# Kernel optimization log

Hardware: AMD Instinct MI355X
Metric: run time of the kernel (lower is better)

Reference implementation:

```python
import jax, jax.numpy as jnp
import numpy as np

WH, WW = 8, 8
N = WH * WW          # 64 tokens per window
C = 128              # channels
H = 4                # heads
HD = C // H          # head dim = 32
B = 4096             # batch * num_windows
NW = 1024            # windows per image (mask groups)
EPS = 1e-5


def _relative_position_index():
    ch = np.arange(WH)
    cw = np.arange(WW)
    coords = np.stack(np.meshgrid(ch, cw, indexing='ij'))        # (2, WH, WW)
    cf = coords.reshape(2, -1)                                    # (2, N)
    rel = cf[:, :, None] - cf[:, None, :]                         # (2, N, N)
    rel = rel.transpose(1, 2, 0).copy()                           # (N, N, 2)
    rel[:, :, 0] += WH - 1
    rel[:, :, 1] += WW - 1
    rel[:, :, 0] *= 2 * WW - 1
    return rel.sum(-1).astype(np.int32)                           # (N, N)


def setup_inputs() -> dict:
    key = jax.random.key(0)
    ks = jax.random.split(key, 12)
    s = 0.02
    tbl_size = (2 * WH - 1) * (2 * WW - 1)
    return {
        'x': jax.random.normal(ks[0], (B, N, C), jnp.float32),
        'y': jax.random.normal(ks[1], (B, N, C), jnp.float32),
        'mask': jnp.zeros((NW, N, N), jnp.float32),
        'wqkv1': jax.random.normal(ks[2], (C, 3 * C), jnp.float32) * s,
        'bqkv1': jnp.zeros((3 * C,), jnp.float32),
        'wqkv2': jax.random.normal(ks[3], (C, 3 * C), jnp.float32) * s,
        'bqkv2': jnp.zeros((3 * C,), jnp.float32),
        'tbl1': jax.random.normal(ks[4], (tbl_size, H), jnp.float32) * s,
        'tbl2': jax.random.normal(ks[5], (tbl_size, H), jnp.float32) * s,
        'wproj1': jax.random.normal(ks[6], (C, C), jnp.float32) * s,
        'bproj1': jnp.zeros((C,), jnp.float32),
        'wproj2': jax.random.normal(ks[7], (C, C), jnp.float32) * s,
        'bproj2': jnp.zeros((C,), jnp.float32),
        'g1': jnp.ones((C,), jnp.float32),
        'be1': jnp.zeros((C,), jnp.float32),
        'g2': jnp.ones((C,), jnp.float32),
        'be2': jnp.zeros((C,), jnp.float32),
        'rpi': jnp.asarray(_relative_position_index()),
    }


def _layernorm(x, g, b):
    mu = jnp.mean(x, -1, keepdims=True)
    var = jnp.mean(jnp.square(x - mu), -1, keepdims=True)
    return (x - mu) * jax.lax.rsqrt(var + EPS) * g + b


def _qkv(t, w, b):
    q, k, v = jnp.split((t @ w + b).reshape(B, N, 3, H, HD).transpose(2, 0, 3, 1, 4), 3, axis=0)
    return q[0], k[0], v[0]


def reference(x, y, mask, wqkv1, bqkv1, wqkv2, bqkv2, tbl1, tbl2,
              wproj1, bproj1, wproj2, bproj2, g1, be1, g2, be2, rpi):
    q1, k1, v1 = _qkv(x, wqkv1, bqkv1)
    q2, k2, v2 = _qkv(y, wqkv2, bqkv2)
    scale = 1.0 / jnp.sqrt(jnp.float32(C))

    bias1 = tbl1[rpi].transpose(2, 0, 1)   # (H, N, N) gathered from small table
    bias2 = tbl2[rpi].transpose(2, 0, 1)

    attn1 = jnp.einsum('bhnd,bhmd->bhnm', q1, k2) * scale + bias1[None]
    attn2 = jnp.einsum('bhnd,bhmd->bhnm', q2, k1) * scale + bias2[None]

    nW = mask.shape[0]
    attn1 = (attn1.reshape(B // nW, nW, H, N, N) + mask[None, :, None]).reshape(B, H, N, N)
    attn2 = (attn2.reshape(B // nW, nW, H, N, N) + mask[None, :, None]).reshape(B, H, N, N)

    attn1 = jax.nn.softmax(attn1, axis=-1)
    attn2 = jax.nn.softmax(attn2, axis=-1)

    out1 = jnp.einsum('bhnm,bhmd->bhnd', attn1, v2).transpose(0, 2, 1, 3).reshape(B, N, C)
    out2 = jnp.einsum('bhnm,bhmd->bhnd', attn2, v1).transpose(0, 2, 1, 3).reshape(B, N, C)

    out1 = _layernorm(out1 @ wproj1 + bproj1 + x, g1, be1)
    out2 = _layernorm(out2 @ wproj2 + bproj2 + y, g2, be2)
    return out1, out2
```

## Files before the change

kernel.cpp:

```cpp
#include <hip/hip_runtime.h>
#include <stdint.h>


typedef __attribute__((ext_vector_type(8))) short short8;
typedef __attribute__((ext_vector_type(4))) short short4v;
typedef __attribute__((ext_vector_type(4))) float f32x4;
typedef __attribute__((ext_vector_type(2))) unsigned int uint2v;

#define MFMA(a, b, c) __builtin_amdgcn_mfma_f32_16x16x32_bf16((a), (b), (c), 0, 0, 0)

static __device__ __forceinline__ unsigned short f2bf(float f) {
  union { float f; uint32_t u; } v; v.f = f;
  uint32_t u = v.u + (0x7fffu + ((v.u >> 16) & 1u));
  return (unsigned short)(u >> 16);
}
static __device__ __forceinline__ uint32_t pk2(float a, float b) {
  return (uint32_t)f2bf(a) | ((uint32_t)f2bf(b) << 16);
}

__global__ __launch_bounds__(256) void prep_kernel(
    const float* __restrict__ wqkv1, const float* __restrict__ wqkv2,
    const float* __restrict__ wproj1, const float* __restrict__ wproj2,
    const float* __restrict__ tbl1, const float* __restrict__ tbl2,
    const int* __restrict__ rpi,
    unsigned short* __restrict__ wq1p, unsigned short* __restrict__ wq2p,
    unsigned short* __restrict__ wp1p, unsigned short* __restrict__ wp2p,
    float* __restrict__ bias1, float* __restrict__ bias2) {
  int tid = blockIdx.x * 256 + threadIdx.x;
  if (tid < 12288) {
    const float* W = (tid < 6144) ? wqkv1 : wqkv2;
    unsigned short* P = (tid < 6144) ? wq1p : wq2p;
    int local = (tid < 6144) ? tid : tid - 6144;
    int tile = local >> 6, lane = local & 63;
    int nt = tile >> 2, kt = tile & 3;
    int n = nt * 16 + (lane & 15);
    int kb = kt * 32 + (lane >> 4) * 8;
    unsigned short* dst = P + (size_t)(tile * 64 + lane) * 8;
#pragma unroll
    for (int j = 0; j < 8; ++j) dst[j] = f2bf(W[(kb + j) * 384 + n]);
  } else if (tid < 16384) {
    int local = tid - 12288;
    const float* W = (local < 2048) ? wproj1 : wproj2;
    unsigned short* P = (local < 2048) ? wp1p : wp2p;
    local &= 2047;
    int tile = local >> 6, lane = local & 63;
    int nt = tile >> 2, kt = tile & 3;
    int n = nt * 16 + (lane & 15);
    int kb = kt * 32 + (lane >> 4) * 8;
    unsigned short* dst = P + (size_t)(tile * 64 + lane) * 8;
#pragma unroll
    for (int j = 0; j < 8; ++j) dst[j] = f2bf(W[(kb + j) * 128 + n]);
  } else if (tid < 49152) {
    int local = tid - 16384;
    const float* T = (local < 16384) ? tbl1 : tbl2;
    float* D = (local < 16384) ? bias1 : bias2;
    local &= 16383;
    int r = local & 3;
    int ln = (local >> 2) & 63;
    int mt = (local >> 8) & 3;
    int ni = (local >> 10) & 3;
    int h = local >> 12;
    int i = ni * 16 + (ln & 15);
    int j = mt * 16 + (ln >> 4) * 4 + r;
    D[local] = T[rpi[i * 64 + j] * 4 + h];
  }
}

__global__ __launch_bounds__(512, 4) void wca_kernel(
    const float* __restrict__ x, const float* __restrict__ y,
    const float* __restrict__ mask,
    const float* __restrict__ bqkv1, const float* __restrict__ bqkv2,
    const float* __restrict__ bproj1, const float* __restrict__ bproj2,
    const float* __restrict__ g1, const float* __restrict__ be1,
    const float* __restrict__ g2, const float* __restrict__ be2,
    const unsigned short* __restrict__ wq1p, const unsigned short* __restrict__ wq2p,
    const unsigned short* __restrict__ wp1p, const unsigned short* __restrict__ wp2p,
    const float* __restrict__ biasT1, const float* __restrict__ biasT2,
    float* __restrict__ out) {
  __shared__ __align__(16) unsigned short sQ[2][4][64][36];
  __shared__ __align__(16) unsigned short sK[2][4][64][40];

  const int b = blockIdx.x;
  const int tid = (int)threadIdx.x;
  const int wave = tid >> 6;
  const int lane = tid & 63;
  const int quad = lane >> 4;
  const int col = lane & 15;
  const int sideA = wave >> 2;
  const int ntg = wave & 3;

  uint32_t vpkA[2][2][2], vpkB[2][2][2];

  {
    const float* src = (sideA ? y : x) + (size_t)b * 8192;
    const unsigned short* wp = sideA ? wq2p : wq1p;
    const float* bq = sideA ? bqkv2 : bqkv1;

#pragma unroll 1
    for (int mh = 0; mh < 2; ++mh) {
      short8 afrag[2][4];
#pragma unroll
      for (int mi = 0; mi < 2; ++mi) {
        int m = (mh * 2 + mi) * 16 + col;
#pragma unroll
        for (int ks = 0; ks < 4; ++ks) {
          const float* p = src + m * 128 + ks * 32 + quad * 8;
          float4 lo = *(const float4*)(p);
          float4 hi4 = *(const float4*)(p + 4);
          short8 f;
          f[0] = (short)f2bf(lo.x); f[1] = (short)f2bf(lo.y);
          f[2] = (short)f2bf(lo.z); f[3] = (short)f2bf(lo.w);
          f[4] = (short)f2bf(hi4.x); f[5] = (short)f2bf(hi4.y);
          f[6] = (short)f2bf(hi4.z); f[7] = (short)f2bf(hi4.w);
          afrag[mi][ks] = f;
        }
      }

#pragma unroll 1
      for (int t = 0; t < 4; ++t) {
        int nt = ntg + t * 4;
        float bias = bq[nt * 16 + col];
        short8 bfrag[4];
#pragma unroll
        for (int ks = 0; ks < 4; ++ks)
          bfrag[ks] = *(const short8*)(wp + (size_t)((nt * 4 + ks) * 64 + lane) * 8);
        int cw = (nt & 7) * 16 + col;
        int hq = cw >> 5, d = cw & 31;
#pragma unroll
        for (int mi = 0; mi < 2; ++mi) {
          f32x4 acc = {bias, bias, bias, bias};
#pragma unroll
          for (int ks = 0; ks < 4; ++ks) acc = MFMA(afrag[mi][ks], bfrag[ks], acc);
#pragma unroll
          for (int r = 0; r < 4; ++r) {
            int row = (mh * 2 + mi) * 16 + quad * 4 + r;
            unsigned short v = f2bf(acc[r]);
            if (t < 2) sQ[sideA][hq][row][d] = v;
            else       sK[sideA][hq][row][d] = v;
          }
        }
      }

#pragma unroll
      for (int vt = 0; vt < 2; ++vt) {
        int nt = ntg + 16 + vt * 4;
        float bias = bq[nt * 16 + col];
        short8 bfrag[4];
#pragma unroll
        for (int ks = 0; ks < 4; ++ks)
          bfrag[ks] = *(const short8*)(wp + (size_t)((nt * 4 + ks) * 64 + lane) * 8);
#pragma unroll
        for (int mi = 0; mi < 2; ++mi) {
          f32x4 acc = {bias, bias, bias, bias};
#pragma unroll
          for (int ks = 0; ks < 4; ++ks) acc = MFMA(afrag[mi][ks], bfrag[ks], acc);
          if (mh == 0) {
            vpkA[vt][mi][0] = pk2(acc[0], acc[1]);
            vpkA[vt][mi][1] = pk2(acc[2], acc[3]);
          } else {
            vpkB[vt][mi][0] = pk2(acc[0], acc[1]);
            vpkB[vt][mi][1] = pk2(acc[2], acc[3]);
          }
        }
      }
    }
  }
  __syncthreads();

  {
    const float scale = 0.08838834764831845f;
    const int h = wave & 3;
    const int qh = wave >> 2;
    const float* mbase = mask + (size_t)(b & 1023) * 4096;
    const int g0 = ((2 * quad) & 3) * 16 + col;
    const int g1 = ((2 * quad + 1) & 3) * 16 + col;
    const int hi = quad >> 1;

#pragma unroll 1
    for (int s = 0; s < 2; ++s) {
      const float* bL = (s == 0 ? biasT1 : biasT2) + h * 4096;

      f32x4 sv[2][4];
      {
        short8 kf[4];
#pragma unroll
        for (int mt = 0; mt < 4; ++mt)
          kf[mt] = *(const short8*)&sK[1 - s][h][mt * 16 + col][quad * 8];
        short8 qf[2];
#pragma unroll
        for (int ni = 0; ni < 2; ++ni) {
          const short4v* qp = (const short4v*)&sQ[s][h][(qh * 2 + ni) * 16 + col][0];
          short4v qa = qp[2 * quad], qb = qp[2 * quad + 1];
          qf[ni] = __builtin_shufflevector(qa, qb, 0, 1, 2, 3, 4, 5, 6, 7);
        }
#pragma unroll
        for (int ni = 0; ni < 2; ++ni)
#pragma unroll
          for (int mt = 0; mt < 4; ++mt) {
            f32x4 z = {0.f, 0.f, 0.f, 0.f};
            sv[ni][mt] = MFMA(kf[mt], qf[ni], z);
          }
      }

#pragma unroll
      for (int ni = 0; ni < 2; ++ni)
#pragma unroll
        for (int mt = 0; mt < 4; ++mt) {
          f32x4 bb = *(const f32x4*)(bL + (size_t)(((qh * 2 + ni) * 4 + mt) * 64 + lane) * 4);
          f32x4 mm = *(const f32x4*)(mbase + ((qh * 2 + ni) * 16 + col) * 64 + mt * 16 + quad * 4);
#pragma unroll
          for (int r = 0; r < 4; ++r)
            sv[ni][mt][r] = fmaf(sv[ni][mt][r], scale, bb[r] + mm[r]);
        }

      __syncthreads();
      if (sideA == 1 - s) {
        unsigned short* vbw = &sK[1 - s][0][0][0];
#pragma unroll
        for (int vt = 0; vt < 2; ++vt) {
          int nt = ntg + 16 + vt * 4;
          int cw = (nt & 7) * 16 + col;
          int hv = cw >> 5, dv = cw & 31;
#pragma unroll
          for (int mt = 0; mt < 4; ++mt) {
            uint2v vv;
            if (mt < 2) { vv.x = vpkA[vt][mt][0];     vv.y = vpkA[vt][mt][1]; }
            else        { vv.x = vpkB[vt][mt - 2][0]; vv.y = vpkB[vt][mt - 2][1]; }
            *(uint2v*)(vbw + hv * 2304 + dv * 72 + mt * 16 + quad * 4) = vv;
          }
        }
      }
      __syncthreads();

      uint32_t pk[2][4][2];
#pragma unroll
      for (int ni = 0; ni < 2; ++ni) {
        float mx = sv[ni][0][0];
#pragma unroll
        for (int mt = 0; mt < 4; ++mt)
#pragma unroll
          for (int r = 0; r < 4; ++r) mx = fmaxf(mx, sv[ni][mt][r]);
        mx = fmaxf(mx, __shfl_xor(mx, 16));
        mx = fmaxf(mx, __shfl_xor(mx, 32));
        float sum = 0.f;
#pragma unroll
        for (int mt = 0; mt < 4; ++mt)
#pragma unroll
          for (int r = 0; r < 4; ++r) {
            float e = __expf(sv[ni][mt][r] - mx);
            sv[ni][mt][r] = e;
            sum += e;
          }
        sum += __shfl_xor(sum, 16);
        sum += __shfl_xor(sum, 32);
        float inv = 1.0f / sum;
#pragma unroll
        for (int mt = 0; mt < 4; ++mt) {
          pk[ni][mt][0] = pk2(sv[ni][mt][0] * inv, sv[ni][mt][1] * inv);
          pk[ni][mt][1] = pk2(sv[ni][mt][2] * inv, sv[ni][mt][3] * inv);
        }
      }

      const unsigned short* vb = &sK[1 - s][0][0][0];
      short8 vf[2][2];
#pragma unroll
      for (int dt = 0; dt < 2; ++dt)
#pragma unroll
        for (int ks = 0; ks < 2; ++ks)
          vf[dt][ks] = *(const short8*)(vb + h * 2304 + (dt * 16 + col) * 72 + ks * 32 + quad * 8);

      short8 af[2][2];
#pragma unroll
      for (int ni = 0; ni < 2; ++ni)
#pragma unroll
        for (int ks = 0; ks < 2; ++ks) {
          union { uint32_t u[4]; short8 v8; } w;
          uint32_t alo, ahi;
          alo = (uint32_t)__shfl((int)pk[ni][2 * ks][0], g0);
          ahi = (uint32_t)__shfl((int)pk[ni][2 * ks + 1][0], g0);
          w.u[0] = hi ? ahi : alo;
          alo = (uint32_t)__shfl((int)pk[ni][2 * ks][1], g0);
          ahi = (uint32_t)__shfl((int)pk[ni][2 * ks + 1][1], g0);
          w.u[1] = hi ? ahi : alo;
          alo = (uint32_t)__shfl((int)pk[ni][2 * ks][0], g1);
          ahi = (uint32_t)__shfl((int)pk[ni][2 * ks + 1][0], g1);
          w.u[2] = hi ? ahi : alo;
          alo = (uint32_t)__shfl((int)pk[ni][2 * ks][1], g1);
          ahi = (uint32_t)__shfl((int)pk[ni][2 * ks + 1][1], g1);
          w.u[3] = hi ? ahi : alo;
          af[ni][ks] = w.v8;
        }

      unsigned short* ob = &sQ[s][0][0][0];
#pragma unroll
      for (int ni = 0; ni < 2; ++ni)
#pragma unroll
        for (int dt = 0; dt < 2; ++dt) {
          f32x4 o = {0.f, 0.f, 0.f, 0.f};
          o = MFMA(af[ni][0], vf[dt][0], o);
          o = MFMA(af[ni][1], vf[dt][1], o);
#pragma unroll
          for (int r = 0; r < 4; ++r)
            ob[((qh * 2 + ni) * 16 + quad * 4 + r) * 136 + h * 32 + dt * 16 + col] = f2bf(o[r]);
        }
    }
  }
  __syncthreads();

  {
    const int side = wave >> 2;
    const int mt = wave & 3;
    const unsigned short* sO = &sQ[side][0][0][0];
    const unsigned short* wpp = side ? wp2p : wp1p;
    const float* bp = side ? bproj2 : bproj1;
    const float* gg = side ? g2 : g1;
    const float* bb = side ? be2 : be1;
    const float* res = (side ? y : x) + (size_t)b * 8192;
    float* o = out + (size_t)side * 33554432 + (size_t)b * 8192;

    short8 af[4];
#pragma unroll
    for (int ks = 0; ks < 4; ++ks)
      af[ks] = *(const short8*)&sO[(mt * 16 + col) * 136 + ks * 32 + quad * 8];

    float vals[8][4];
#pragma unroll
    for (int nt = 0; nt < 8; ++nt) {
      float bias = bp[nt * 16 + col];
      f32x4 acc = {bias, bias, bias, bias};
#pragma unroll
      for (int ks = 0; ks < 4; ++ks)
        acc = MFMA(af[ks], *(const short8*)(wpp + (size_t)((nt * 4 + ks) * 64 + lane) * 8), acc);
#pragma unroll
      for (int r = 0; r < 4; ++r)
        vals[nt][r] = acc[r] + res[(mt * 16 + quad * 4 + r) * 128 + nt * 16 + col];
    }

#pragma unroll
    for (int r = 0; r < 4; ++r) {
      float sum = 0.f;
#pragma unroll
      for (int nt = 0; nt < 8; ++nt) sum += vals[nt][r];
      sum += __shfl_xor(sum, 1, 16);
      sum += __shfl_xor(sum, 2, 16);
      sum += __shfl_xor(sum, 4, 16);
      sum += __shfl_xor(sum, 8, 16);
      float mean = sum * 0.0078125f;
      float vsum = 0.f;
#pragma unroll
      for (int nt = 0; nt < 8; ++nt) {
        float dd = vals[nt][r] - mean;
        vsum += dd * dd;
      }
      vsum += __shfl_xor(vsum, 1, 16);
      vsum += __shfl_xor(vsum, 2, 16);
      vsum += __shfl_xor(vsum, 4, 16);
      vsum += __shfl_xor(vsum, 8, 16);
      float rstd = rsqrtf(vsum * 0.0078125f + 1e-5f);
      int row = mt * 16 + quad * 4 + r;
#pragma unroll
      for (int nt = 0; nt < 8; ++nt) {
        int c = nt * 16 + col;
        o[row * 128 + c] = (vals[nt][r] - mean) * rstd * gg[c] + bb[c];
      }
    }
  }
}

extern "C" void kernel_launch(void* const* d_in, const int* in_sizes, int n_in,
                              void* d_out, int out_size, void* d_ws, size_t ws_size,
                              hipStream_t stream) {
  const float* x = (const float*)d_in[0];
  const float* y = (const float*)d_in[1];
  const float* mask = (const float*)d_in[2];
  const float* wqkv1 = (const float*)d_in[3];
  const float* bqkv1 = (const float*)d_in[4];
  const float* wqkv2 = (const float*)d_in[5];
  const float* bqkv2 = (const float*)d_in[6];
  const float* tbl1 = (const float*)d_in[7];
  const float* tbl2 = (const float*)d_in[8];
  const float* wproj1 = (const float*)d_in[9];
  const float* bproj1 = (const float*)d_in[10];
  const float* wproj2 = (const float*)d_in[11];
  const float* bproj2 = (const float*)d_in[12];
  const float* g1 = (const float*)d_in[13];
  const float* be1 = (const float*)d_in[14];
  const float* g2 = (const float*)d_in[15];
  const float* be2 = (const float*)d_in[16];
  const int* rpi = (const int*)d_in[17];

  char* ws = (char*)d_ws;
  unsigned short* wq1p = (unsigned short*)(ws + 0);
  unsigned short* wq2p = (unsigned short*)(ws + 98304);
  unsigned short* wp1p = (unsigned short*)(ws + 196608);
  unsigned short* wp2p = (unsigned short*)(ws + 229376);
  float* bias1 = (float*)(ws + 262144);
  float* bias2 = (float*)(ws + 327680);

  prep_kernel<<<dim3(192), dim3(256), 0, stream>>>(
      wqkv1, wqkv2, wproj1, wproj2, tbl1, tbl2, rpi,
      wq1p, wq2p, wp1p, wp2p, bias1, bias2);

  wca_kernel<<<dim3(4096), dim3(512), 0, stream>>>(
      x, y, mask, bqkv1, bqkv2, bproj1, bproj2,
      g1, be1, g2, be2, wq1p, wq2p, wp1p, wp2p, bias1, bias2,
      (float*)d_out);
}
```

Baseline: 840.9 us.

## Preload Q/K fragments for both sides and cut per-side barriers in attention

All K and Q fragments for both attention directions are now loaded into registers up front. Both V halves are then written into the freed K buffers in a single phase. This replaces the four barriers inside the side loop with two barriers before it. The side loop is fully unrolled and processes one query tile (ni) at a time, which shrinks live score registers but holds more K/Q fragment registers for the whole loop.

```diff
diff --git a/kernel.cpp b/kernel.cpp
--- a/kernel.cpp
+++ b/kernel.cpp
@@ -176,70 +176,74 @@
     const int g1 = ((2 * quad + 1) & 3) * 16 + col;
     const int hi = quad >> 1;
 
-#pragma unroll 1
+    short8 kf[2][4];
+    short8 qf[2][2];
+#pragma unroll
+    for (int s = 0; s < 2; ++s) {
+#pragma unroll
+      for (int mt = 0; mt < 4; ++mt)
+        kf[s][mt] = *(const short8*)&sK[1 - s][h][mt * 16 + col][quad * 8];
+#pragma unroll
+      for (int ni = 0; ni < 2; ++ni) {
+        const short4v* qp = (const short4v*)&sQ[s][h][(qh * 2 + ni) * 16 + col][0];
+        short4v qa = qp[2 * quad], qb = qp[2 * quad + 1];
+        qf[s][ni] = __builtin_shufflevector(qa, qb, 0, 1, 2, 3, 4, 5, 6, 7);
+      }
+    }
+    __syncthreads();
+
+    {
+      unsigned short* vbw = &sK[sideA][0][0][0];
+#pragma unroll
+      for (int vt = 0; vt < 2; ++vt) {
+        int nt = ntg + 16 + vt * 4;
+        int cw = (nt & 7) * 16 + col;
+        int hv = cw >> 5, dv = cw & 31;
+#pragma unroll
+        for (int mt = 0; mt < 4; ++mt) {
+          uint2v vv;
+          if (mt < 2) { vv.x = vpkA[vt][mt][0];     vv.y = vpkA[vt][mt][1]; }
+          else        { vv.x = vpkB[vt][mt - 2][0]; vv.y = vpkB[vt][mt - 2][1]; }
+          *(uint2v*)(vbw + hv * 2304 + dv * 72 + mt * 16 + quad * 4) = vv;
+        }
+      }
+    }
+    __syncthreads();
+
+#pragma unroll
     for (int s = 0; s < 2; ++s) {
       const float* bL = (s == 0 ? biasT1 : biasT2) + h * 4096;
-
-      f32x4 sv[2][4];
-      {
-        short8 kf[4];
-#pragma unroll
-        for (int mt = 0; mt < 4; ++mt)
-          kf[mt] = *(const short8*)&sK[1 - s][h][mt * 16 + col][quad * 8];
-        short8 qf[2];
-#pragma unroll
-        for (int ni = 0; ni < 2; ++ni) {
-          const short4v* qp = (const short4v*)&sQ[s][h][(qh * 2 + ni) * 16 + col][0];
-          short4v qa = qp[2 * quad], qb = qp[2 * quad + 1];
-          qf[ni] = __builtin_shufflevector(qa, qb, 0, 1, 2, 3, 4, 5, 6, 7);
-        }
-#pragma unroll
-        for (int ni = 0; ni < 2; ++ni)
-#pragma unroll
-          for (int mt = 0; mt < 4; ++mt) {
-            f32x4 z = {0.f, 0.f, 0.f, 0.f};
-            sv[ni][mt] = MFMA(kf[mt], qf[ni], z);
-          }
-      }
-
-#pragma unroll
-      for (int ni = 0; ni < 2; ++ni)
+      const unsigned short* vb = &sK[1 - s][0][0][0];
+      unsigned short* ob = &sQ[s][0][0][0];
+
+      short8 vf[2][2];
+#pragma unroll
+      for (int dt = 0; dt < 2; ++dt)
+#pragma unroll
+        for (int ks = 0; ks < 2; ++ks)
+          vf[dt][ks] = *(const short8*)(vb + h * 2304 + (dt * 16 + col) * 72 + ks * 32 + quad * 8);
+
+#pragma unroll
+      for (int ni = 0; ni < 2; ++ni) {
+        f32x4 sv[4];
+#pragma unroll
+        for (int mt = 0; mt < 4; ++mt) {
+          f32x4 z = {0.f, 0.f, 0.f, 0.f};
+          sv[mt] = MFMA(kf[s][mt], qf[s][ni], z);
+        }
 #pragma unroll
         for (int mt = 0; mt < 4; ++mt) {
           f32x4 bb = *(const f32x4*)(bL + (size_t)(((qh * 2 + ni) * 4 + mt) * 64 + lane) * 4);
           f32x4 mm = *(const f32x4*)(mbase + ((qh * 2 + ni) * 16 + col) * 64 + mt * 16 + quad * 4);
 #pragma unroll
           for (int r = 0; r < 4; ++r)
-            sv[ni][mt][r] = fmaf(sv[ni][mt][r], scale, bb[r] + mm[r]);
-        }
-
-      __syncthreads();
-      if (sideA == 1 - s) {
-        unsigned short* vbw = &sK[1 - s][0][0][0];
-#pragma unroll
-        for (int vt = 0; vt < 2; ++vt) {
-          int nt = ntg + 16 + vt * 4;
-          int cw = (nt & 7) * 16 + col;
-          int hv = cw >> 5, dv = cw & 31;
-#pragma unroll
-          for (int mt = 0; mt < 4; ++mt) {
-            uint2v vv;
-            if (mt < 2) { vv.x = vpkA[vt][mt][0];     vv.y = vpkA[vt][mt][1]; }
-            else        { vv.x = vpkB[vt][mt - 2][0]; vv.y = vpkB[vt][mt - 2][1]; }
-            *(uint2v*)(vbw + hv * 2304 + dv * 72 + mt * 16 + quad * 4) = vv;
-          }
-        }
-      }
-      __syncthreads();
-
-      uint32_t pk[2][4][2];
-#pragma unroll
-      for (int ni = 0; ni < 2; ++ni) {
-        float mx = sv[ni][0][0];
+            sv[mt][r] = fmaf(sv[mt][r], scale, bb[r] + mm[r]);
+        }
+        float mx = sv[0][0];
 #pragma unroll
         for (int mt = 0; mt < 4; ++mt)
 #pragma unroll
-          for (int r = 0; r < 4; ++r) mx = fmaxf(mx, sv[ni][mt][r]);
+          for (int r = 0; r < 4; ++r) mx = fmaxf(mx, sv[mt][r]);
         mx = fmaxf(mx, __shfl_xor(mx, 16));
         mx = fmaxf(mx, __shfl_xor(mx, 32));
         float sum = 0.f;
@@ -247,62 +251,48 @@
         for (int mt = 0; mt < 4; ++mt)
 #pragma unroll
           for (int r = 0; r < 4; ++r) {
-            float e = __expf(sv[ni][mt][r] - mx);
-            sv[ni][mt][r] = e;
+            float e = __expf(sv[mt][r] - mx);
+            sv[mt][r] = e;
             sum += e;
           }
         sum += __shfl_xor(sum, 16);
         sum += __shfl_xor(sum, 32);
         float inv = 1.0f / sum;
+        uint32_t pk[4][2];
 #pragma unroll
         for (int mt = 0; mt < 4; ++mt) {
-          pk[ni][mt][0] = pk2(sv[ni][mt][0] * inv, sv[ni][mt][1] * inv);
-          pk[ni][mt][1] = pk2(sv[ni][mt][2] * inv, sv[ni][mt][3] * inv);
-        }
-      }
-
-      const unsigned short* vb = &sK[1 - s][0][0][0];
-      short8 vf[2][2];
-#pragma unroll
-      for (int dt = 0; dt < 2; ++dt)
-#pragma unroll
-        for (int ks = 0; ks < 2; ++ks)
-          vf[dt][ks] = *(const short8*)(vb + h * 2304 + (dt * 16 + col) * 72 + ks * 32 + quad * 8);
-
-      short8 af[2][2];
-#pragma unroll
-      for (int ni = 0; ni < 2; ++ni)
+          pk[mt][0] = pk2(sv[mt][0] * inv, sv[mt][1] * inv);
+          pk[mt][1] = pk2(sv[mt][2] * inv, sv[mt][3] * inv);
+        }
+        short8 af[2];
 #pragma unroll
         for (int ks = 0; ks < 2; ++ks) {
           union { uint32_t u[4]; short8 v8; } w;
           uint32_t alo, ahi;
-          alo = (uint32_t)__shfl((int)pk[ni][2 * ks][0], g0);
-          ahi = (uint32_t)__shfl((int)pk[ni][2 * ks + 1][0], g0);
+          alo = (uint32_t)__shfl((int)pk[2 * ks][0], g0);
+          ahi = (uint32_t)__shfl((int)pk[2 * ks + 1][0], g0);
           w.u[0] = hi ? ahi : alo;
-          alo = (uint32_t)__shfl((int)pk[ni][2 * ks][1], g0);
-          ahi = (uint32_t)__shfl((int)pk[ni][2 * ks + 1][1], g0);
+          alo = (uint32_t)__shfl((int)pk[2 * ks][1], g0);
+          ahi = (uint32_t)__shfl((int)pk[2 * ks + 1][1], g0);
           w.u[1] = hi ? ahi : alo;
-          alo = (uint32_t)__shfl((int)pk[ni][2 * ks][0], g1);
-          ahi = (uint32_t)__shfl((int)pk[ni][2 * ks + 1][0], g1);
+          alo = (uint32_t)__shfl((int)pk[2 * ks][0], g1);
+          ahi = (uint32_t)__shfl((int)pk[2 * ks + 1][0], g1);
           w.u[2] = hi ? ahi : alo;
-          alo = (uint32_t)__shfl((int)pk[ni][2 * ks][1], g1);
-          ahi = (uint32_t)__shfl((int)pk[ni][2 * ks + 1][1], g1);
+          alo = (uint32_t)__shfl((int)pk[2 * ks][1], g1);
+          ahi = (uint32_t)__shfl((int)pk[2 * ks + 1][1], g1);
           w.u[3] = hi ? ahi : alo;
-          af[ni][ks] = w.v8;
-        }
-
-      unsigned short* ob = &sQ[s][0][0][0];
-#pragma unroll
-      for (int ni = 0; ni < 2; ++ni)
+          af[ks] = w.v8;
+        }
 #pragma unroll
         for (int dt = 0; dt < 2; ++dt) {
           f32x4 o = {0.f, 0.f, 0.f, 0.f};
-          o = MFMA(af[ni][0], vf[dt][0], o);
-          o = MFMA(af[ni][1], vf[dt][1], o);
+          o = MFMA(af[0], vf[dt][0], o);
+          o = MFMA(af[1], vf[dt][1], o);
 #pragma unroll
           for (int r = 0; r < 4; ++r)
             ob[((qh * 2 + ni) * 16 + quad * 4 + r) * 136 + h * 32 + dt * 16 + col] = f2bf(o[r]);
         }
+      }
     }
   }
   __syncthreads();
```

Result: no change. 846.6 us (+0.7%).
